# Optimization experiments

Measured on AMD Instinct MI355X. Metric: run time of the kernel, lower is better.

The kernel has to match this reference:

```python
import jax, jax.numpy as jnp
import numpy as np

TAG_SIZE = 50
START = TAG_SIZE - 2  # index of '<START>'
STOP = TAG_SIZE - 1   # index of '<STOP>'
B, S = 64, 512


def setup_inputs() -> dict:
    key = jax.random.key(0)
    k1, k2, k3 = jax.random.split(key, 3)
    feats = jax.random.normal(k1, (B, S, TAG_SIZE), dtype=jnp.float32)
    mask = jnp.ones((B, S), dtype=jnp.int32)
    tags = jax.random.randint(k2, (B, S), 0, START)  # valid tags exclude START/STOP
    transitions = jax.random.normal(k3, (TAG_SIZE, TAG_SIZE), dtype=jnp.float32)
    return {"feats": feats, "mask": mask, "tags": tags, "transitions": transitions}


def reference(feats, mask, tags, transitions):
    """CRF neg_log_likelihood_loss = forward_score (log partition, summed) - gold_score.
    feats: (B,S,T) emissions; mask: (B,S) {0,1}; tags: (B,S) gold tags;
    transitions[i,j] = score of transitioning from tag i to tag j.
    """
    b, s, t = feats.shape
    maskf = mask.astype(feats.dtype)

    # ---- forward algorithm (log partition) via scan over time ----
    feats_t = jnp.swapaxes(feats, 0, 1)            # (S,B,T)
    mask_t = jnp.swapaxes(mask, 0, 1).astype(bool)  # (S,B)
    # t=0: partition[b,j] = feats[b,0,j] + transitions[START, j]
    partition0 = feats_t[0] + transitions[START][None, :]  # (B,T)

    def step(partition, xs):
        f_t, m_t = xs  # (B,T), (B,)
        # cur_values[b,i,j] = partition[b,i] + transitions[i,j] + feats[b,t,j]
        cur_values = partition[:, :, None] + transitions[None, :, :] + f_t[:, None, :]
        cur = jax.nn.logsumexp(cur_values, axis=1)  # (B,T) logsumexp over prev tag
        new_partition = jnp.where(m_t[:, None], cur, partition)
        return new_partition, None

    partition, _ = jax.lax.scan(step, partition0, (feats_t[1:], mask_t[1:]))
    terminal = jax.nn.logsumexp(partition[:, :, None] + transitions[None, :, :], axis=1)  # (B,T)
    forward_score = terminal[:, STOP].sum()

    # ---- gold score ----
    # prev tag at step 0 is START, otherwise tags[:, t-1]
    prev = jnp.concatenate([jnp.full((b, 1), START, dtype=tags.dtype), tags[:, :-1]], axis=1)
    emit = jnp.take_along_axis(feats, tags[..., None], axis=2)[..., 0]  # (B,S)
    trans = transitions[prev, tags]                                      # (B,S)
    tg_energy = ((emit + trans) * maskf).sum()
    lengths = mask.astype(jnp.int32).sum(axis=1)                         # (B,)
    end_ids = jnp.take_along_axis(tags, (lengths - 1)[:, None].astype(tags.dtype), axis=1)[:, 0]
    end_energy = transitions[end_ids, STOP].sum()
    gold_score = tg_energy + end_energy

    return forward_score - gold_score
```

## Files before the change

### kernel.cpp

```cpp
#include <hip/hip_runtime.h>
#include <hip/hip_bf16.h>

#define T 50
#define NB 64
#define NS 512
#define START_TAG 48
#define STOP_TAG 49

typedef _Float16 f16_t;
typedef _Float16 f16x2 __attribute__((ext_vector_type(2)));
typedef _Float16 f16x4 __attribute__((ext_vector_type(4)));
typedef _Float16 f16x8 __attribute__((ext_vector_type(8)));
typedef float    f32x4 __attribute__((ext_vector_type(4)));

static constexpr float LOG2E = 1.4426950408889634f;
static constexpr float LN2F  = 0.6931471805599453f;
static constexpr float S_E   = 6.0f;
#define NEG_BIG (-1.0e38f)

__device__ __forceinline__ float fexp2(float x) { return __builtin_amdgcn_exp2f(x); }
__device__ __forceinline__ float flog2(float x) { return __builtin_amdgcn_logf(x); }
__device__ __forceinline__ f16x2 bcast_h2(f16x2 v, int src) {
    unsigned u = __builtin_amdgcn_readlane(__builtin_bit_cast(unsigned, v), src);
    return __builtin_bit_cast(f16x2, u);
}
__device__ __forceinline__ f16x2 pack_h2(float a, float b) {
    return __builtin_bit_cast(f16x2, __builtin_amdgcn_cvt_pkrtz(a, b));
}

__device__ __forceinline__ float wave_fmax_dpp(float x) {
#define DPP_STEP(ctrl)                                                        \
    do {                                                                      \
        int _s = __builtin_bit_cast(int, x);                                  \
        int _p = __builtin_amdgcn_update_dpp(_s, _s, (ctrl), 0xf, 0xf, false);\
        x = fmaxf(x, __builtin_bit_cast(float, _p));                          \
    } while (0)
    DPP_STEP(0x111);
    DPP_STEP(0x112);
    DPP_STEP(0x114);
    DPP_STEP(0x118);
    DPP_STEP(0x142);
    DPP_STEP(0x143);
#undef DPP_STEP
    return __builtin_bit_cast(float,
        __builtin_amdgcn_readlane(__builtin_bit_cast(int, x), 63));
}

template<int NCHT, int CHLT>
__global__ __launch_bounds__(256, 8)
void crf_chunk(const float* __restrict__ feats, const int* __restrict__ mask,
               const float* __restrict__ trans, f16_t* __restrict__ wsCt,
               float* __restrict__ wsD, float* __restrict__ out, int out_size) {
    const int c    = blockIdx.x;
    const int b    = blockIdx.y;
    const int tid  = threadIdx.x;
    const int w    = tid >> 6;
    const int lane = tid & 63;
    const int l15  = lane & 15;
    const int q    = lane >> 4;

    constexpr int EF_BYTES = 4 * 2 * 64 * 16;
    constexpr int SF_BYTES = CHLT * 64 * 4;
    constexpr int ML_BYTES = 64 * 72 * 2;
    constexpr int SM_BYTES = (EF_BYTES + SF_BYTES) > ML_BYTES
                           ? (EF_BYTES + SF_BYTES) : ML_BYTES;
    __shared__ unsigned char smem[SM_BYTES];
    f16_t* Ef = (f16_t*)smem;
    float (*sF)[64] = (float (*)[64])(smem + EF_BYTES);

    const int t0  = c * CHLT + 1;
    const int nst = (NS - t0 < CHLT) ? (NS - t0) : CHLT;

    for (int sidx = tid; sidx < 512; sidx += 256) {
        const int kb  = sidx >> 7;
        const int mbp = (sidx >> 6) & 1;
        const int ln  = sidx & 63;
        const int qq  = ln >> 4;
        const int ll  = ln & 15;
        f16_t* slot = Ef + sidx * 8;
        #pragma unroll
        for (int e = 0; e < 2; e++)
            #pragma unroll
            for (int j = 0; j < 4; j++) {
                const int kk = 16 * kb + 4 * qq + j;
                const int mm = 16 * (2 * mbp + e) + ll;
                float x = 0.f;
                if (kk < T && mm < T) x = fexp2(fmaf(trans[kk * T + mm], LOG2E, -S_E));
                slot[e * 4 + j] = (f16_t)x;
            }
    }

    for (int r = w; r < CHLT; r += 4) {
        int tl = t0 + r; tl = tl < NS ? tl : NS - 1;
        float fv = (lane < T && r < nst) ? feats[((size_t)b * NS + tl) * T + lane] : 0.f;
        sF[r][lane] = (lane < T && r < nst) ? fexp2(fv * LOG2E) : 0.f;
    }

    unsigned long long bm;
    {
        int tl = t0 + lane; tl = tl < NS ? tl : NS - 1;
        int mv = (lane < nst) ? mask[b * NS + tl] : 0;
        bm = __ballot(mv != 0);
    }
    __syncthreads();

    f16x4 Bt[4];
    #pragma unroll
    for (int rb = 0; rb < 4; rb++) {
        f16x4 v;
        #pragma unroll
        for (int j = 0; j < 4; j++)
            v[j] = (f16_t)((rb == w && 4 * q + j == l15) ? 1.f : 0.f);
        Bt[rb] = v;
    }

    float D  = 0.f;
    float m1 = 1.f, m2 = 1.f;
    const f16x8* EfL = (const f16x8*)Ef;

    for (int s = 0; s < nst; s++) {
        if ((bm >> s) & 1ull) {
            int ebits = (int)((__float_as_uint(m2) >> 23) & 255) - 127;
            ebits = ebits > 14 ? 14 : (ebits < -14 ? -14 : ebits);
            const float descale = __uint_as_float((unsigned)(127 - ebits) << 23);
            D += (float)ebits + S_E;

            const f32x4 zz = {0.f, 0.f, 0.f, 0.f};
            f32x4 acc[4];
            {
                f16x8 p0 = EfL[0 * 64 + lane];
                f16x8 p1 = EfL[1 * 64 + lane];
                acc[0] = __builtin_amdgcn_mfma_f32_16x16x16f16(__builtin_shufflevector(p0, p0, 0,1,2,3), Bt[0], zz, 0, 0, 0);
                acc[1] = __builtin_amdgcn_mfma_f32_16x16x16f16(__builtin_shufflevector(p0, p0, 4,5,6,7), Bt[0], zz, 0, 0, 0);
                acc[2] = __builtin_amdgcn_mfma_f32_16x16x16f16(__builtin_shufflevector(p1, p1, 0,1,2,3), Bt[0], zz, 0, 0, 0);
                acc[3] = __builtin_amdgcn_mfma_f32_16x16x16f16(__builtin_shufflevector(p1, p1, 4,5,6,7), Bt[0], zz, 0, 0, 0);
            }
            #pragma unroll
            for (int kb = 1; kb < 4; kb++) {
                f16x8 p0 = EfL[(kb * 2 + 0) * 64 + lane];
                f16x8 p1 = EfL[(kb * 2 + 1) * 64 + lane];
                acc[0] = __builtin_amdgcn_mfma_f32_16x16x16f16(__builtin_shufflevector(p0, p0, 0,1,2,3), Bt[kb], acc[0], 0, 0, 0);
                acc[1] = __builtin_amdgcn_mfma_f32_16x16x16f16(__builtin_shufflevector(p0, p0, 4,5,6,7), Bt[kb], acc[1], 0, 0, 0);
                acc[2] = __builtin_amdgcn_mfma_f32_16x16x16f16(__builtin_shufflevector(p1, p1, 0,1,2,3), Bt[kb], acc[2], 0, 0, 0);
                acc[3] = __builtin_amdgcn_mfma_f32_16x16x16f16(__builtin_shufflevector(p1, p1, 4,5,6,7), Bt[kb], acc[3], 0, 0, 0);
            }

            f16x2 wmax2 = {(f16_t)0.f, (f16_t)0.f};
            #pragma unroll
            for (int mb = 0; mb < 4; mb++) {
                f32x4 cs = *(const f32x4*)&sF[s][16 * mb + 4 * q];
                float v0 = acc[mb][0] * (cs[0] * descale);
                float v1 = acc[mb][1] * (cs[1] * descale);
                float v2 = acc[mb][2] * (cs[2] * descale);
                float v3 = acc[mb][3] * (cs[3] * descale);
                f16x4 hv;
                hv[0] = (f16_t)v0; hv[1] = (f16_t)v1;
                hv[2] = (f16_t)v2; hv[3] = (f16_t)v3;
                Bt[mb] = hv;
                f16x2 lo = __builtin_shufflevector(hv, hv, 0, 1);
                f16x2 hi = __builtin_shufflevector(hv, hv, 2, 3);
                wmax2 = __builtin_elementwise_max(wmax2,
                          __builtin_elementwise_max(lo, hi));
            }
            float wm = fmaxf((float)wmax2[0], (float)wmax2[1]);

            m2 = m1;
            m1 = wave_fmax_dpp(wm);
        }
    }

    __syncthreads();
    {
        f16_t* Ml = (f16_t*)smem;
        const int P2 = 72;
        #pragma unroll
        for (int rb = 0; rb < 4; rb++) {
            f16x4 v = Bt[rb];
            #pragma unroll
            for (int r = 0; r < 4; r++)
                Ml[(16 * rb + 4 * q + r) * P2 + 16 * w + l15] = v[r];
        }
        __syncthreads();
        const int row = tid >> 2;
        const int seg = tid & 3;
        const f16_t* src = &Ml[row * P2 + seg * 16];
        f16_t* dst = wsCt + ((size_t)(b * NCHT + c)) * 4096 + row * 64 + seg * 16;
        ((int4*)dst)[0] = *(const int4*)&src[0];
        ((int4*)dst)[1] = *(const int4*)&src[8];
    }
    if (lane == 0) wsD[(b * NCHT + c) * 4 + w] = D;

    if (c == 0 && b == 0 && tid < out_size) out[tid] = 0.f;
}

template<int NCHT>
__global__ __launch_bounds__(128, 1)
void crf_combine(const float* __restrict__ feats, const int* __restrict__ mask,
                 const int* __restrict__ tags, const float* __restrict__ trans,
                 const f16_t* __restrict__ wsCt, const float* __restrict__ wsD,
                 float* __restrict__ out) {
    const int b    = blockIdx.x;
    const int tid  = threadIdx.x;
    const int wv   = tid >> 6;
    const int lane = tid & 63;

    __shared__ float sGold;
    float fwd = 0.f;

    if (wv == 1) {
        float gsum = 0.f;
        int   lcnt = 0;
        for (int s = lane; s < NS; s += 64) {
            int   m  = mask[b * NS + s];
            int   tg = tags[b * NS + s];
            int   pv = (s == 0) ? START_TAG : tags[b * NS + s - 1];
            float e  = feats[((size_t)b * NS + s) * T + tg];
            float tr = trans[pv * T + tg];
            if (m) { gsum += e + tr; lcnt += 1; }
        }
        #pragma unroll
        for (int off = 32; off > 0; off >>= 1) {
            gsum += __shfl_down(gsum, off, 64);
            lcnt += __shfl_down(lcnt, off, 64);
        }
        if (lane == 0) sGold = gsum + trans[tags[b * NS + lcnt - 1] * T + STOP_TAG];
    } else {
        float part = (lane < T)
            ? (feats[(size_t)b * NS * T + lane] + trans[START_TAG * T + lane]) * LOG2E
            : NEG_BIG;

        float Dq[NCHT];
        #pragma unroll
        for (int cc = 0; cc < NCHT; cc++)
            Dq[cc] = wsD[(b * NCHT + cc) * 4 + (lane >> 4)];

        int bX[32], bY[32], bZ[32];

        auto ld = [&](int (&buf)[32], int cc) {
            const f16_t* src = wsCt + (size_t)(b * NCHT + cc) * 4096 + lane * 64;
            #pragma unroll
            for (int kk = 0; kk < 8; kk++)
                *(int4*)&buf[4 * kk] = ((const int4*)src)[kk];
        };

        auto body = [&](int (&cur)[32], int cc) {
            float tmp = part + Dq[cc];
            float sft = wave_fmax_dpp(tmp);
            float ex  = fexp2(tmp - sft);
            float exo = __shfl_xor(ex, 1, 64);
            f16x2 pk  = pack_h2(ex, exo);

            float a0 = 0.f, a1 = 0.f, a2 = 0.f, a3 = 0.f;
            #pragma unroll
            for (int k = 0; k < 25; k += 4) {
                a0 = __builtin_amdgcn_fdot2(bcast_h2(pk, 2 * k), __builtin_bit_cast(f16x2, cur[k]), a0, false);
                if (k + 1 < 25) a1 = __builtin_amdgcn_fdot2(bcast_h2(pk, 2 * (k + 1)), __builtin_bit_cast(f16x2, cur[k + 1]), a1, false);
                if (k + 2 < 25) a2 = __builtin_amdgcn_fdot2(bcast_h2(pk, 2 * (k + 2)), __builtin_bit_cast(f16x2, cur[k + 2]), a2, false);
                if (k + 3 < 25) a3 = __builtin_amdgcn_fdot2(bcast_h2(pk, 2 * (k + 3)), __builtin_bit_cast(f16x2, cur[k + 3]), a3, false);
            }
            part = sft + flog2((a0 + a1) + (a2 + a3));
        };

        ld(bX, 0);
        if (1 < NCHT) ld(bY, 1);
        #pragma unroll
        for (int g = 0; g < NCHT; g += 3) {
            { if (g + 2 < NCHT) ld(bZ, g + 2); body(bX, g); }
            if (g + 1 < NCHT) { if (g + 3 < NCHT) ld(bX, g + 3); body(bY, g + 1); }
            if (g + 2 < NCHT) { if (g + 4 < NCHT) ld(bY, g + 4); body(bZ, g + 2); }
        }

        float v = (lane < T) ? part + trans[lane * T + STOP_TAG] * LOG2E : NEG_BIG;
        float mx = wave_fmax_dpp(v);
        float ee = (lane < T) ? fexp2(v - mx) : 0.f;
        #pragma unroll
        for (int off = 32; off > 0; off >>= 1) ee += __shfl_xor(ee, off, 64);
        fwd = (mx + flog2(ee)) * LN2F;
    }

    __syncthreads();
    if (tid == 0) atomicAdd(out, fwd - sGold);
}

extern "C" void kernel_launch(void* const* d_in, const int* in_sizes, int n_in,
                              void* d_out, int out_size, void* d_ws, size_t ws_size,
                              hipStream_t stream) {
    const float* feats = (const float*)d_in[0];
    const int*   mask  = (const int*)d_in[1];
    const int*   tags  = (const int*)d_in[2];
    const float* trans = (const float*)d_in[3];
    float* out = (float*)d_out;


    const size_t matBytes16 = (size_t)NB * 16 * 4096 * sizeof(f16_t);
    const size_t need16     = matBytes16 + (size_t)NB * 16 * 4 * sizeof(float);

    if (ws_size >= need16) {
        f16_t* wsCt = (f16_t*)d_ws;
        float* wsD  = (float*)((char*)d_ws + matBytes16);
        crf_chunk<16, 32><<<dim3(16, NB), 256, 0, stream>>>(feats, mask, trans, wsCt, wsD, out, out_size);
        crf_combine<16><<<NB, 128, 0, stream>>>(feats, mask, tags, trans, wsCt, wsD, out);
    } else {
        const size_t matBytes8 = (size_t)NB * 8 * 4096 * sizeof(f16_t);
        f16_t* wsCt = (f16_t*)d_ws;
        float* wsD  = (float*)((char*)d_ws + matBytes8);
        crf_chunk<8, 64><<<dim3(8, NB), 256, 0, stream>>>(feats, mask, trans, wsCt, wsD, out, out_size);
        crf_combine<8><<<NB, 128, 0, stream>>>(feats, mask, tags, trans, wsCt, wsD, out);
    }
}
```

Measured before the change: 106.6 us.

## Keep half of transition matrix in registers and split sequence into 32 chunks

The first two k-blocks of the exponentiated transition matrix are now held as MFMA A-fragments in registers, so each step reads only the remaining half from LDS, which halves the LDS footprint for that matrix. When the workspace is large enough, the launch also prefers 32 chunks of 16 steps per batch over 16 chunks of 32. Shorter chunks shorten the serial per-block recurrence and double the grid, but they add more chunk matrices to write to the workspace and a longer serial combine, and the extra register fragments may reduce occupancy.

Result: slower. 110.7 us (+3.9%).

```diff
diff --git a/kernel.cpp b/kernel.cpp
--- a/kernel.cpp
+++ b/kernel.cpp
@@ -59,7 +59,7 @@
     const int l15  = lane & 15;
     const int q    = lane >> 4;
 
-    constexpr int EF_BYTES = 4 * 2 * 64 * 16;
+    constexpr int EF_BYTES = 2 * 2 * 64 * 16;
     constexpr int SF_BYTES = CHLT * 64 * 4;
     constexpr int ML_BYTES = 64 * 72 * 2;
     constexpr int SM_BYTES = (EF_BYTES + SF_BYTES) > ML_BYTES
@@ -71,8 +71,26 @@
     const int t0  = c * CHLT + 1;
     const int nst = (NS - t0 < CHLT) ? (NS - t0) : CHLT;
 
-    for (int sidx = tid; sidx < 512; sidx += 256) {
-        const int kb  = sidx >> 7;
+    f16x4 Afr[2][4];
+    #pragma unroll
+    for (int kb = 0; kb < 2; kb++)
+        #pragma unroll
+        for (int mb = 0; mb < 4; mb++) {
+            f16x4 v;
+            #pragma unroll
+            for (int j = 0; j < 4; j++) {
+                const int kk = 16 * kb + 4 * q + j;
+                const int mm = 16 * mb + l15;
+                float x = 0.f;
+                if (kk < T && mm < T) x = fexp2(fmaf(trans[kk * T + mm], LOG2E, -S_E));
+                v[j] = (f16_t)x;
+            }
+            Afr[kb][mb] = v;
+        }
+
+    {
+        const int sidx = tid;
+        const int kbr = sidx >> 7;
         const int mbp = (sidx >> 6) & 1;
         const int ln  = sidx & 63;
         const int qq  = ln >> 4;
@@ -82,7 +100,7 @@
         for (int e = 0; e < 2; e++)
             #pragma unroll
             for (int j = 0; j < 4; j++) {
-                const int kk = 16 * kb + 4 * qq + j;
+                const int kk = 16 * (kbr + 2) + 4 * qq + j;
                 const int mm = 16 * (2 * mbp + e) + ll;
                 float x = 0.f;
                 if (kk < T && mm < T) x = fexp2(fmaf(trans[kk * T + mm], LOG2E, -S_E));
@@ -127,22 +145,20 @@
 
             const f32x4 zz = {0.f, 0.f, 0.f, 0.f};
             f32x4 acc[4];
-            {
-                f16x8 p0 = EfL[0 * 64 + lane];
-                f16x8 p1 = EfL[1 * 64 + lane];
-                acc[0] = __builtin_amdgcn_mfma_f32_16x16x16f16(__builtin_shufflevector(p0, p0, 0,1,2,3), Bt[0], zz, 0, 0, 0);
-                acc[1] = __builtin_amdgcn_mfma_f32_16x16x16f16(__builtin_shufflevector(p0, p0, 4,5,6,7), Bt[0], zz, 0, 0, 0);
-                acc[2] = __builtin_amdgcn_mfma_f32_16x16x16f16(__builtin_shufflevector(p1, p1, 0,1,2,3), Bt[0], zz, 0, 0, 0);
-                acc[3] = __builtin_amdgcn_mfma_f32_16x16x16f16(__builtin_shufflevector(p1, p1, 4,5,6,7), Bt[0], zz, 0, 0, 0);
-            }
-            #pragma unroll
-            for (int kb = 1; kb < 4; kb++) {
-                f16x8 p0 = EfL[(kb * 2 + 0) * 64 + lane];
-                f16x8 p1 = EfL[(kb * 2 + 1) * 64 + lane];
-                acc[0] = __builtin_amdgcn_mfma_f32_16x16x16f16(__builtin_shufflevector(p0, p0, 0,1,2,3), Bt[kb], acc[0], 0, 0, 0);
-                acc[1] = __builtin_amdgcn_mfma_f32_16x16x16f16(__builtin_shufflevector(p0, p0, 4,5,6,7), Bt[kb], acc[1], 0, 0, 0);
-                acc[2] = __builtin_amdgcn_mfma_f32_16x16x16f16(__builtin_shufflevector(p1, p1, 0,1,2,3), Bt[kb], acc[2], 0, 0, 0);
-                acc[3] = __builtin_amdgcn_mfma_f32_16x16x16f16(__builtin_shufflevector(p1, p1, 4,5,6,7), Bt[kb], acc[3], 0, 0, 0);
+            #pragma unroll
+            for (int mb = 0; mb < 4; mb++)
+                acc[mb] = __builtin_amdgcn_mfma_f32_16x16x16f16(Afr[0][mb], Bt[0], zz, 0, 0, 0);
+            #pragma unroll
+            for (int mb = 0; mb < 4; mb++)
+                acc[mb] = __builtin_amdgcn_mfma_f32_16x16x16f16(Afr[1][mb], Bt[1], acc[mb], 0, 0, 0);
+            #pragma unroll
+            for (int kbr = 0; kbr < 2; kbr++) {
+                f16x8 p0 = EfL[(kbr * 2 + 0) * 64 + lane];
+                f16x8 p1 = EfL[(kbr * 2 + 1) * 64 + lane];
+                acc[0] = __builtin_amdgcn_mfma_f32_16x16x16f16(__builtin_shufflevector(p0, p0, 0,1,2,3), Bt[2 + kbr], acc[0], 0, 0, 0);
+                acc[1] = __builtin_amdgcn_mfma_f32_16x16x16f16(__builtin_shufflevector(p0, p0, 4,5,6,7), Bt[2 + kbr], acc[1], 0, 0, 0);
+                acc[2] = __builtin_amdgcn_mfma_f32_16x16x16f16(__builtin_shufflevector(p1, p1, 0,1,2,3), Bt[2 + kbr], acc[2], 0, 0, 0);
+                acc[3] = __builtin_amdgcn_mfma_f32_16x16x16f16(__builtin_shufflevector(p1, p1, 4,5,6,7), Bt[2 + kbr], acc[3], 0, 0, 0);
             }
 
             f16x2 wmax2 = {(f16_t)0.f, (f16_t)0.f};
@@ -292,10 +308,17 @@
     float* out = (float*)d_out;
 
 
+    const size_t matBytes32 = (size_t)NB * 32 * 4096 * sizeof(f16_t);
+    const size_t need32     = matBytes32 + (size_t)NB * 32 * 4 * sizeof(float);
     const size_t matBytes16 = (size_t)NB * 16 * 4096 * sizeof(f16_t);
     const size_t need16     = matBytes16 + (size_t)NB * 16 * 4 * sizeof(float);
 
-    if (ws_size >= need16) {
+    if (ws_size >= need32) {
+        f16_t* wsCt = (f16_t*)d_ws;
+        float* wsD  = (float*)((char*)d_ws + matBytes32);
+        crf_chunk<32, 16><<<dim3(32, NB), 256, 0, stream>>>(feats, mask, trans, wsCt, wsD, out, out_size);
+        crf_combine<32><<<NB, 128, 0, stream>>>(feats, mask, tags, trans, wsCt, wsD, out);
+    } else if (ws_size >= need16) {
         f16_t* wsCt = (f16_t*)d_ws;
         float* wsD  = (float*)((char*)d_ws + matBytes16);
         crf_chunk<16, 32><<<dim3(16, NB), 256, 0, stream>>>(feats, mask, trans, wsCt, wsD, out, out_size);
```
